# Kernel optimization log

Measured on AMD Instinct MI355X. Metric: run time of the kernel, lower is better.

Reference implementation:

```python
import jax, jax.numpy as jnp
import numpy as np

B, L, D, W = 4, 512, 768, 12
K = L * W  # number of candidate spans


def _mlp(x, w1, b1, w2, b2):
    # Linear -> ReLU -> (Dropout=identity in eval) -> Linear
    return jax.nn.relu(x @ w1.T + b1) @ w2.T + b2


def setup_inputs() -> dict:
    key = jax.random.key(0)
    ks = jax.random.split(key, 16)
    sc_d = 1.0 / np.sqrt(D)
    sc_4d = 1.0 / np.sqrt(4 * D)
    sc_2d = 1.0 / np.sqrt(2 * D)
    inp = {
        "h": jax.random.normal(ks[0], (B, L, D), dtype=jnp.float32),
        "span_idx": jax.random.randint(ks[1], (B, K, 2), 0, L, dtype=jnp.int64),
        # project_start: Linear(D,4D), Linear(4D,D)
        "ws1": jax.random.uniform(ks[2], (4 * D, D), jnp.float32, -sc_d, sc_d),
        "bs1": jax.random.uniform(ks[3], (4 * D,), jnp.float32, -sc_d, sc_d),
        "ws2": jax.random.uniform(ks[4], (D, 4 * D), jnp.float32, -sc_4d, sc_4d),
        "bs2": jax.random.uniform(ks[5], (D,), jnp.float32, -sc_4d, sc_4d),
        # project_end
        "we1": jax.random.uniform(ks[6], (4 * D, D), jnp.float32, -sc_d, sc_d),
        "be1": jax.random.uniform(ks[7], (4 * D,), jnp.float32, -sc_d, sc_d),
        "we2": jax.random.uniform(ks[8], (D, 4 * D), jnp.float32, -sc_4d, sc_4d),
        "be2": jax.random.uniform(ks[9], (D,), jnp.float32, -sc_4d, sc_4d),
        # out_project: Linear(2D,4D), Linear(4D,D)
        "wo1": jax.random.uniform(ks[10], (4 * D, 2 * D), jnp.float32, -sc_2d, sc_2d),
        "bo1": jax.random.uniform(ks[11], (4 * D,), jnp.float32, -sc_2d, sc_2d),
        "wo2": jax.random.uniform(ks[12], (D, 4 * D), jnp.float32, -sc_4d, sc_4d),
        "bo2": jax.random.uniform(ks[13], (D,), jnp.float32, -sc_4d, sc_4d),
    }
    return inp


def reference(h, span_idx, ws1, bs1, ws2, bs2, we1, be1, we2, be2, wo1, bo1, wo2, bo2):
    start_rep = _mlp(h, ws1, bs1, ws2, bs2)  # [B, L, D]
    end_rep = _mlp(h, we1, be1, we2, be2)    # [B, L, D]
    bidx = jnp.arange(B)[:, None]
    start_span = start_rep[bidx, span_idx[:, :, 0]]  # gather along seq dim -> [B, K, D]
    end_span = end_rep[bidx, span_idx[:, :, 1]]      # [B, K, D]
    cat = jax.nn.relu(jnp.concatenate([start_span, end_span], axis=-1))  # [B, K, 2D]
    out = _mlp(cat, wo1, bo1, wo2, bo2)  # [B, K, D]
    return out.reshape(B, L, W, D)
```

## Files before the change

kernel.cpp:

```cpp
#include <hip/hip_runtime.h>
#include <hip/hip_bf16.h>

using bf16 = __hip_bfloat16;
using bf16x8 = __attribute__((ext_vector_type(8))) __bf16;
using f32x4  = __attribute__((ext_vector_type(4))) float;
using u32x4  = __attribute__((ext_vector_type(4))) unsigned;
typedef unsigned short ushort_t;

#define BM 128
#define BN 128
#define BK 32


__device__ __forceinline__ void gl_lds16(const void* g, void* l) {
  __builtin_amdgcn_global_load_lds(
      (const __attribute__((address_space(1))) void*)g,
      (__attribute__((address_space(3))) void*)l, 16, 0, 0);
}

__device__ __forceinline__ ushort_t f2bf(float f) {
  unsigned u = __float_as_uint(f);
  u += 0x7FFF + ((u >> 16) & 1);
  return (ushort_t)(u >> 16);
}

__global__ void sniff(const unsigned* __restrict__ w1,
                      const unsigned* __restrict__ idx, int* flags) {
  __shared__ int cnt[2];
  if (threadIdx.x == 0) { cnt[0] = 0; cnt[1] = 0; }
  __syncthreads();
  int t = threadIdx.x;
  int c0 = 0;
  for (int k = 0; k < 4; ++k) {
    unsigned lo = w1[t * 4 + k] & 0xFFFFu;
    unsigned e = (lo >> 7) & 0xFF;
    if (e <= 122) c0++;
  }
  int c1 = (idx[2 * t + 1] != 0) ? 1 : 0;
  atomicAdd(&cnt[0], c0);
  atomicAdd(&cnt[1], c1);
  __syncthreads();
  if (threadIdx.x == 0) {
    flags[0] = (cnt[0] >= 900) ? 1 : 0;
    flags[1] = (cnt[1] == 0) ? 1 : 0;
  }
}

__global__ void norm_idx(const int* __restrict__ flags, const void* __restrict__ src,
                         int* __restrict__ dst) {
  int i = blockIdx.x * 256 + threadIdx.x;
  int v = flags[1] ? (int)((const long long*)src)[i] : ((const int*)src)[i];
  dst[i] = v;
}

__global__ void cvt_all(const int* __restrict__ flags,
                        const void* s0, const void* s1, const void* s2,
                        const void* s3, const void* s4, const void* s5,
                        const void* s6, ushort_t* __restrict__ dst) {
  long i = ((long)blockIdx.x * 256 + threadIdx.x) * 4;
  const void* src; long off;
  if      (i <  1572864) { src = s0; off = i; }
  else if (i <  3932160) { src = s1; off = i - 1572864; }
  else if (i <  6291456) { src = s2; off = i - 3932160; }
  else if (i <  8650752) { src = s3; off = i - 6291456; }
  else if (i < 11010048) { src = s4; off = i - 8650752; }
  else if (i < 15728640) { src = s5; off = i - 11010048; }
  else                   { src = s6; off = i - 15728640; }
  if (flags[0]) {
    *(ushort4*)(dst + i) = *((const ushort4*)((const ushort_t*)src + off));
  } else {
    float4 f = ((const float4*)src)[off >> 2];
    ushort4 o;
    o.x = f2bf(f.x); o.y = f2bf(f.y); o.z = f2bf(f.z); o.w = f2bf(f.w);
    *(ushort4*)(dst + i) = o;
  }
}

__global__ void cvt_bias(const int* __restrict__ flags,
                         const void* b0, const void* b1, const void* b2,
                         const void* b3, const void* b4, const void* b5,
                         float* __restrict__ dst) {
  int i = blockIdx.x * 256 + threadIdx.x;
  if (i >= 14592) return;
  if (i >= 11520) { dst[i] = 0.f; return; }
  const void* src; int off;
  if (i < 3072)       { src = b0; off = i; }
  else if (i < 3840)  { src = b1; off = i - 3072; }
  else if (i < 6912)  { src = b2; off = i - 3840; }
  else if (i < 7680)  { src = b3; off = i - 6912; }
  else if (i < 10752) { src = b4; off = i - 7680; }
  else                { src = b5; off = i - 10752; }
  dst[i] = flags[0] ? __bfloat162float(((const bf16*)src)[off])
                    : ((const float*)src)[off];
}

template <bool GATHER, bool RELU, bool OUTF32>
__global__ __launch_bounds__(256) void gemm_bt(
    const bf16* __restrict__ A, const bf16* __restrict__ A2,
    const bf16* __restrict__ repS, const bf16* __restrict__ repE,
    const int* __restrict__ sidx, int row_base,
    const bf16* __restrict__ Bw, const bf16* __restrict__ Bw2,
    const float* __restrict__ bias, const float* __restrict__ bias2,
    void* __restrict__ C, void* __restrict__ C2, int nsplit,
    int N, int Kdim, int bstride) {
  __shared__ bf16 lA[BM * BK];
  __shared__ bf16 lB[BN * BK];

  const int tid  = threadIdx.x;
  const int lane = tid & 63;
  const int wave = tid >> 6;
  const int wm = wave >> 1, wn = wave & 1;
  int by = blockIdx.y;
  const bf16* Bw_ = Bw; const float* bias_ = bias; void* C_ = C; const bf16* A_ = A;
  if (by >= nsplit) { by -= nsplit; Bw_ = Bw2; bias_ = bias2; C_ = C2; A_ = A2; }
  const int m0 = blockIdx.x * BM;
  const int n0 = by * BN;

  const int srow = tid >> 2;
  const int scol = 8 * ((tid & 3) ^ ((tid >> 3) & 3));

  const bf16 *a0 = nullptr, *a1 = nullptr;
  const bf16 *pS0 = nullptr, *pE0 = nullptr, *pS1 = nullptr, *pE1 = nullptr;
  if (GATHER) {
    int r0 = row_base + m0 + srow;
    int r1 = r0 + 64;
    int b0 = r0 / 6144, b1 = r1 / 6144;
    int s0 = min(max(sidx[2 * r0], 0), 511);
    int e0 = min(max(sidx[2 * r0 + 1], 0), 511);
    int s1 = min(max(sidx[2 * r1], 0), 511);
    int e1 = min(max(sidx[2 * r1 + 1], 0), 511);
    pS0 = repS + ((size_t)b0 * 512 + s0) * 768 + scol;
    pE0 = repE + ((size_t)b0 * 512 + e0) * 768 + scol;
    pS1 = repS + ((size_t)b1 * 512 + s1) * 768 + scol;
    pE1 = repE + ((size_t)b1 * 512 + e1) * 768 + scol;
  } else {
    a0 = A_ + (size_t)(m0 + srow) * Kdim + scol;
    a1 = a0 + (size_t)64 * Kdim;
  }
  const bf16* b0p = Bw_ + (size_t)(n0 + srow) * bstride + scol;
  const bf16* b1p = b0p + (size_t)64 * bstride;

  f32x4 acc[4][4];
  const f32x4 z = {0.f, 0.f, 0.f, 0.f};
#pragma unroll
  for (int i = 0; i < 4; ++i)
#pragma unroll
    for (int j = 0; j < 4; ++j) acc[i][j] = z;

  const int fr = lane & 15;
  const int fk = 8 * ((lane >> 4) ^ ((lane >> 1) & 3));

  for (int k0 = 0; k0 < Kdim; k0 += BK) {
    const bf16 *sa0, *sa1;
    if (GATHER) {
      if (k0 < 768) { sa0 = pS0 + k0; sa1 = pS1 + k0; }
      else          { sa0 = pE0 + (k0 - 768); sa1 = pE1 + (k0 - 768); }
    } else {
      sa0 = a0 + k0; sa1 = a1 + k0;
    }
    gl_lds16(sa0, lA + tid * 8);
    gl_lds16(sa1, lA + 2048 + tid * 8);
    gl_lds16(b0p + k0, lB + tid * 8);
    gl_lds16(b1p + k0, lB + 2048 + tid * 8);
    __syncthreads();

    bf16x8 af[4], bv[4];
#pragma unroll
    for (int i = 0; i < 4; ++i)
      af[i] = *(const bf16x8*)(const void*)(lA + (wm * 64 + i * 16 + fr) * BK + fk);
#pragma unroll
    for (int j = 0; j < 4; ++j)
      bv[j] = *(const bf16x8*)(const void*)(lB + (wn * 64 + j * 16 + fr) * BK + fk);
#pragma unroll
    for (int i = 0; i < 4; ++i)
#pragma unroll
      for (int j = 0; j < 4; ++j)
        acc[i][j] = __builtin_amdgcn_mfma_f32_16x16x32_bf16(af[i], bv[j], acc[i][j], 0, 0, 0);
    __syncthreads();
  }

  float* Cf = (float*)C_;
  bf16*  Cb = (bf16*)C_;
#pragma unroll
  for (int j = 0; j < 4; ++j) {
    int n = n0 + wn * 64 + j * 16 + fr;
    float bj = bias_[n];
#pragma unroll
    for (int i = 0; i < 4; ++i) {
      int mb = m0 + wm * 64 + i * 16 + (lane >> 4) * 4;
#pragma unroll
      for (int r = 0; r < 4; ++r) {
        float v = acc[i][j][r] + bj;
        if (RELU) v = fmaxf(v, 0.f);
        if (OUTF32) Cf[(size_t)(mb + r) * N + n] = v;
        else        Cb[(size_t)(mb + r) * N + n] = __float2bfloat16(v);
      }
    }
  }
}

__global__ __launch_bounds__(512) void gemm_final_fused(
    const ushort_t* __restrict__ Ps, const ushort_t* __restrict__ Pe,
    const int* __restrict__ sidx,
    const bf16* __restrict__ Bw, const float* __restrict__ bias,
    float* __restrict__ out) {
  __shared__ bf16 lA[2 * 2048];
  __shared__ bf16 lB[2 * 12288];

  const int tid  = threadIdx.x;
  const int lane = tid & 63;
  const int wave = tid >> 6;
  const int m0 = blockIdx.x * 64;
  const int n0 = blockIdx.y * 384;

  const int srow = tid >> 2;
  const int scol = 8 * ((tid & 3) ^ ((tid >> 3) & 3));

  const ushort_t *pS0 = nullptr, *pE0 = nullptr;
  if (tid < 256) {
    int r0 = m0 + srow;
    int b0 = r0 / 6144;
    int s0 = min(max(sidx[2 * r0], 0), 511);
    int e0 = min(max(sidx[2 * r0 + 1], 0), 511);
    pS0 = Ps + ((size_t)b0 * 512 + s0) * 3072 + scol;
    pE0 = Pe + ((size_t)b0 * 512 + e0) * 3072 + scol;
  }
  const bf16* bp0 = Bw + (size_t)(n0 +       srow) * 3072 + scol;
  const bf16* bp1 = Bw + (size_t)(n0 + 128 + srow) * 3072 + scol;
  const bf16* bp2 = Bw + (size_t)(n0 + 256 + srow) * 3072 + scol;

  f32x4 acc[4][3];
  const f32x4 z = {0.f, 0.f, 0.f, 0.f};
#pragma unroll
  for (int i = 0; i < 4; ++i)
#pragma unroll
    for (int j = 0; j < 3; ++j) acc[i][j] = z;

  const int fr = lane & 15;
  const int fk = 8 * ((lane >> 4) ^ ((lane >> 1) & 3));

  auto pack_store = [&](u32x4 xs, u32x4 xe, bf16* dst) {
    u32x4 wv;
#pragma unroll
    for (int q = 0; q < 4; ++q) {
      float lo = fmaxf(__uint_as_float(xs[q] << 16) + __uint_as_float(xe[q] << 16), 0.f);
      float hi = fmaxf(__uint_as_float(xs[q] & 0xFFFF0000u) +
                       __uint_as_float(xe[q] & 0xFFFF0000u), 0.f);
      unsigned w;
      asm("v_cvt_pk_bf16_f32 %0, %1, %2" : "=v"(w) : "v"(lo), "v"(hi));
      wv[q] = w;
    }
    *(u32x4*)(void*)dst = wv;
  };

  {
    gl_lds16(bp0, lB + tid * 8);
    gl_lds16(bp1, lB + 4096 + tid * 8);
    gl_lds16(bp2, lB + 8192 + tid * 8);
    if (tid < 256) {
      u32x4 xs = *(const u32x4*)(const void*)pS0;
      u32x4 xe = *(const u32x4*)(const void*)pE0;
      pack_store(xs, xe, lA + tid * 8);
    }
    __syncthreads();
  }

  for (int it = 0; it < 96; ++it) {
    const int curA = (it & 1) << 11;
    const int curB = (it & 1) * 12288;
    const int nxtA = curA ^ 2048;
    const int nxtB = (curB == 0) ? 12288 : 0;
    const int k1 = (it + 1) * BK;
    const bool pre = (it + 1) < 96;
    u32x4 xs, xe;
    if (pre) {
      gl_lds16(bp0 + k1, lB + nxtB + tid * 8);
      gl_lds16(bp1 + k1, lB + nxtB + 4096 + tid * 8);
      gl_lds16(bp2 + k1, lB + nxtB + 8192 + tid * 8);
      if (tid < 256) {
        xs = *(const u32x4*)(const void*)(pS0 + k1);
        xe = *(const u32x4*)(const void*)(pE0 + k1);
      }
    }

    bf16x8 af[4];
#pragma unroll
    for (int i = 0; i < 4; ++i)
      af[i] = *(const bf16x8*)(const void*)(lA + curA + (i * 16 + fr) * BK + fk);
#pragma unroll
    for (int j = 0; j < 3; ++j) {
      const int nb = wave * 48 + j * 16;
      bf16x8 bv = *(const bf16x8*)(const void*)(
          lB + curB + (nb >> 7) * 4096 + ((nb & 127) + fr) * BK + fk);
#pragma unroll
      for (int i = 0; i < 4; ++i)
        acc[i][j] = __builtin_amdgcn_mfma_f32_16x16x32_bf16(af[i], bv, acc[i][j], 0, 0, 0);
    }

    if (pre && tid < 256) {
      pack_store(xs, xe, lA + nxtA + tid * 8);
    }
    __syncthreads();
  }

#pragma unroll
  for (int j = 0; j < 3; ++j) {
    int n = n0 + wave * 48 + j * 16 + fr;
    float bj = bias[n];
#pragma unroll
    for (int i = 0; i < 4; ++i) {
      int mb = m0 + i * 16 + (lane >> 4) * 4;
#pragma unroll
      for (int r = 0; r < 4; ++r)
        out[(size_t)(mb + r) * 768 + n] = acc[i][j][r] + bj;
    }
  }
}

extern "C" void kernel_launch(void* const* d_in, const int* in_sizes, int n_in,
                              void* d_out, int out_size, void* d_ws, size_t ws_size,
                              hipStream_t stream) {
  const void* h    = d_in[0];
  const void* sidx = d_in[1];
  const void *ws1 = d_in[2],  *bs1 = d_in[3];
  const void *ws2 = d_in[4],  *bs2 = d_in[5];
  const void *we1 = d_in[6],  *be1 = d_in[7];
  const void *we2 = d_in[8],  *be2 = d_in[9];
  const void *wo1 = d_in[10], *bo1 = d_in[11];
  const void *wo2 = d_in[12], *bo2 = d_in[13];

  char* p = (char*)d_ws;
  int*      flags = (int*)p;
  int*      idx32 = (int*)(p + 256);
  float*    biasf = (float*)(p + 256 + 196608);
  ushort_t* hb    = (ushort_t*)(p + 256 + 196608 + 65536);
  ushort_t* w1sb  = hb   + (size_t)1572864;
  ushort_t* w2sb  = w1sb + (size_t)2359296;
  ushort_t* w1eb  = w2sb + (size_t)2359296;
  ushort_t* w2eb  = w1eb + (size_t)2359296;
  ushort_t* wo1b  = w2eb + (size_t)2359296;
  ushort_t* wo2b  = wo1b + (size_t)4718592;
  ushort_t* repS  = wo2b + (size_t)2359296;
  ushort_t* repE  = repS + (size_t)1572864;
  char*     R     = (char*)(repE + (size_t)1572864);
  size_t fixed = (size_t)(R - (char*)d_ws);
  if (ws_size < fixed) return;
  size_t Rsz = ws_size - fixed;

  const size_t P_BF = (size_t)2 * 2048 * 3072 * 2;
  int tier = (Rsz >= P_BF) ? 2 : 3;

  dim3 blk(256);
  const int XBIG = 0x40000000;
  sniff<<<1, blk, 0, stream>>>((const unsigned*)ws1, (const unsigned*)sidx, flags);
  norm_idx<<<192, blk, 0, stream>>>(flags, sidx, idx32);
  cvt_all<<<17664, blk, 0, stream>>>(flags, h, ws1, ws2, we1, we2, wo1, wo2, hb);
  cvt_bias<<<57, blk, 0, stream>>>(flags, bs1, bs2, be1, be2, bo1, bo2, biasf);
  const float *bs1f = biasf, *bs2f = biasf + 3072, *be1f = biasf + 3840,
              *be2f = biasf + 6912, *bo1f = biasf + 7680, *bo2f = biasf + 10752,
              *zerof = biasf + 11520;
  float* outf = (float*)d_out;

  if (tier == 2) {
    ushort_t* hidS = (ushort_t*)R;
    ushort_t* hidE = hidS + (size_t)2048 * 3072;
    gemm_bt<false, true, false><<<dim3(16, 48), blk, 0, stream>>>(
        (const bf16*)hb, (const bf16*)hb, nullptr, nullptr, nullptr, 0,
        (const bf16*)w1sb, (const bf16*)w1eb, bs1f, be1f,
        hidS, hidE, 24, 3072, 768, 768);
    gemm_bt<false, true, false><<<dim3(16, 12), blk, 0, stream>>>(
        (const bf16*)hidS, (const bf16*)hidE, nullptr, nullptr, nullptr, 0,
        (const bf16*)w2sb, (const bf16*)w2eb, bs2f, be2f,
        (bf16*)repS, (bf16*)repE, 6, 768, 3072, 3072);
    ushort_t* Ps = (ushort_t*)R;
    ushort_t* Pe = Ps + (size_t)2048 * 3072;
    gemm_bt<false, false, false><<<dim3(16, 48), blk, 0, stream>>>(
        (const bf16*)repS, (const bf16*)repE, nullptr, nullptr, nullptr, 0,
        (const bf16*)wo1b, (const bf16*)wo1b + 768, bo1f, zerof,
        Ps, Pe, 24, 3072, 768, 1536);
    gemm_final_fused<<<dim3(384, 2), dim3(512), 0, stream>>>(
        Ps, Pe, idx32, (const bf16*)wo2b, bo2f, outf);
  } else {
    long long cT = (long long)(Rsz / ((size_t)2 * 3072 * 2));
    cT = (cT / 128) * 128; if (cT > 2048) cT = 2048;
    long long cO = (long long)(Rsz / ((size_t)3072 * 2));
    cO = (cO / 128) * 128; if (cO > 24576) cO = 24576;
    if (cT < 128 || cO < 128) return;
    ushort_t* scr = (ushort_t*)R;
    for (long long r = 0; r < 2048; r += cT) {
      long long mc = 2048 - r < cT ? 2048 - r : cT;
      ushort_t* hidS = scr;
      ushort_t* hidE = scr + (size_t)cT * 3072;
      gemm_bt<false, true, false><<<dim3(mc / 128, 48), blk, 0, stream>>>(
          (const bf16*)hb + r * 768, (const bf16*)hb + r * 768,
          nullptr, nullptr, nullptr, 0,
          (const bf16*)w1sb, (const bf16*)w1eb, bs1f, be1f,
          hidS, hidE, 24, 3072, 768, 768);
      gemm_bt<false, true, false><<<dim3(mc / 128, 12), blk, 0, stream>>>(
          (const bf16*)hidS, (const bf16*)hidE, nullptr, nullptr, nullptr, 0,
          (const bf16*)w2sb, (const bf16*)w2eb, bs2f, be2f,
          (bf16*)repS + r * 768, (bf16*)repE + r * 768, 6, 768, 3072, 3072);
    }
    for (long long r = 0; r < 24576; r += cO) {
      long long mc = 24576 - r < cO ? 24576 - r : cO;
      gemm_bt<true, true, false><<<dim3(mc / 128, 24), blk, 0, stream>>>(
          nullptr, nullptr, (const bf16*)repS, (const bf16*)repE, idx32, (int)r,
          (const bf16*)wo1b, nullptr, bo1f, nullptr,
          scr, nullptr, XBIG, 3072, 1536, 1536);
      gemm_bt<false, false, true><<<dim3(mc / 128, 6), blk, 0, stream>>>(
          (const bf16*)scr, nullptr, nullptr, nullptr, nullptr, 0,
          (const bf16*)wo2b, nullptr, bo2f, nullptr,
          outf + (size_t)r * 768, nullptr, XBIG, 768, 3072, 3072);
    }
  }
}
```

Before: 485.4 us.

## Retile fused final GEMM to 64x256 tiles with BK=64 and 2x4 wave grid

The gather-fused final GEMM moves from 64x384 block tiles with 8 waves along N to 64x256 tiles with a 2x4 wave layout. Each iteration now covers K=64, split into two 32-wide sub-slabs, which halves the number of loop iterations and barriers. All 512 threads now take part in the gather/ReLU/pack staging of A instead of only half of them. The grid grows to 384x3 blocks. The cost is a larger LDS footprint, and each A row is gathered and converted three times instead of twice.

```diff
diff --git a/kernel.cpp b/kernel.cpp
--- a/kernel.cpp
+++ b/kernel.cpp
@@ -204,37 +204,38 @@
     const int* __restrict__ sidx,
     const bf16* __restrict__ Bw, const float* __restrict__ bias,
     float* __restrict__ out) {
-  __shared__ bf16 lA[2 * 2048];
-  __shared__ bf16 lB[2 * 12288];
+  __shared__ bf16 lA[2 * 4096];
+  __shared__ bf16 lB[2 * 16384];
 
   const int tid  = threadIdx.x;
   const int lane = tid & 63;
   const int wave = tid >> 6;
+  const int wm = wave >> 2, wn = wave & 3;
   const int m0 = blockIdx.x * 64;
-  const int n0 = blockIdx.y * 384;
-
-  const int srow = tid >> 2;
-  const int scol = 8 * ((tid & 3) ^ ((tid >> 3) & 3));
-
-  const ushort_t *pS0 = nullptr, *pE0 = nullptr;
-  if (tid < 256) {
-    int r0 = m0 + srow;
-    int b0 = r0 / 6144;
-    int s0 = min(max(sidx[2 * r0], 0), 511);
-    int e0 = min(max(sidx[2 * r0 + 1], 0), 511);
-    pS0 = Ps + ((size_t)b0 * 512 + s0) * 3072 + scol;
-    pE0 = Pe + ((size_t)b0 * 512 + e0) * 3072 + scol;
-  }
-  const bf16* bp0 = Bw + (size_t)(n0 +       srow) * 3072 + scol;
-  const bf16* bp1 = Bw + (size_t)(n0 + 128 + srow) * 3072 + scol;
-  const bf16* bp2 = Bw + (size_t)(n0 + 256 + srow) * 3072 + scol;
-
-  f32x4 acc[4][3];
+  const int n0 = blockIdx.y * 256;
+
+  const int t8   = tid & 255;
+  const int ksub = tid >> 8;
+  const int srow = t8 >> 2;
+  const int scol = 8 * ((t8 & 3) ^ ((t8 >> 3) & 3));
+
+  int r0 = m0 + srow;
+  int b0 = r0 / 6144;
+  int s0 = min(max(sidx[2 * r0], 0), 511);
+  int e0 = min(max(sidx[2 * r0 + 1], 0), 511);
+  const ushort_t* pS0 = Ps + ((size_t)b0 * 512 + s0) * 3072 + ksub * 32 + scol;
+  const ushort_t* pE0 = Pe + ((size_t)b0 * 512 + e0) * 3072 + ksub * 32 + scol;
+  const int aoff = ksub * 2048 + t8 * 8;
+
+  const bf16* bp = Bw + (size_t)(n0 + srow) * 3072 + ksub * 32 + scol;
+  const int boff = ksub * 8192 + t8 * 8;
+
+  f32x4 acc[2][4];
   const f32x4 z = {0.f, 0.f, 0.f, 0.f};
 #pragma unroll
-  for (int i = 0; i < 4; ++i)
-#pragma unroll
-    for (int j = 0; j < 3; ++j) acc[i][j] = z;
+  for (int i = 0; i < 2; ++i)
+#pragma unroll
+    for (int j = 0; j < 4; ++j) acc[i][j] = z;
 
   const int fr = lane & 15;
   const int fk = 8 * ((lane >> 4) ^ ((lane >> 1) & 3));
@@ -253,63 +254,64 @@
     *(u32x4*)(void*)dst = wv;
   };
 
+  auto stageB = [&](int k0, int buf) {
+#pragma unroll
+    for (int g = 0; g < 4; ++g)
+      gl_lds16(bp + (size_t)g * 64 * 3072 + k0, lB + buf + boff + g * 2048);
+  };
+
   {
-    gl_lds16(bp0, lB + tid * 8);
-    gl_lds16(bp1, lB + 4096 + tid * 8);
-    gl_lds16(bp2, lB + 8192 + tid * 8);
-    if (tid < 256) {
-      u32x4 xs = *(const u32x4*)(const void*)pS0;
-      u32x4 xe = *(const u32x4*)(const void*)pE0;
-      pack_store(xs, xe, lA + tid * 8);
-    }
+    stageB(0, 0);
+    u32x4 xs = *(const u32x4*)(const void*)pS0;
+    u32x4 xe = *(const u32x4*)(const void*)pE0;
+    pack_store(xs, xe, lA + aoff);
     __syncthreads();
   }
 
-  for (int it = 0; it < 96; ++it) {
-    const int curA = (it & 1) << 11;
-    const int curB = (it & 1) * 12288;
-    const int nxtA = curA ^ 2048;
-    const int nxtB = (curB == 0) ? 12288 : 0;
-    const int k1 = (it + 1) * BK;
-    const bool pre = (it + 1) < 96;
+  for (int it = 0; it < 48; ++it) {
+    const int curA = (it & 1) << 12;
+    const int curB = (it & 1) << 14;
+    const int nxtA = curA ^ 4096;
+    const int nxtB = curB ^ 16384;
+    const int k1 = (it + 1) * 64;
+    const bool pre = (it + 1) < 48;
     u32x4 xs, xe;
     if (pre) {
-      gl_lds16(bp0 + k1, lB + nxtB + tid * 8);
-      gl_lds16(bp1 + k1, lB + nxtB + 4096 + tid * 8);
-      gl_lds16(bp2 + k1, lB + nxtB + 8192 + tid * 8);
-      if (tid < 256) {
-        xs = *(const u32x4*)(const void*)(pS0 + k1);
-        xe = *(const u32x4*)(const void*)(pE0 + k1);
+      stageB(k1, nxtB);
+      xs = *(const u32x4*)(const void*)(pS0 + k1);
+      xe = *(const u32x4*)(const void*)(pE0 + k1);
+    }
+
+#pragma unroll
+    for (int s = 0; s < 2; ++s) {
+      bf16x8 af[2];
+#pragma unroll
+      for (int i = 0; i < 2; ++i)
+        af[i] = *(const bf16x8*)(const void*)(
+            lA + curA + s * 2048 + (wm * 32 + i * 16 + fr) * 32 + fk);
+#pragma unroll
+      for (int j = 0; j < 4; ++j) {
+        bf16x8 bv = *(const bf16x8*)(const void*)(
+            lB + curB + s * 8192 + (wn * 64 + j * 16 + fr) * 32 + fk);
+#pragma unroll
+        for (int i = 0; i < 2; ++i)
+          acc[i][j] = __builtin_amdgcn_mfma_f32_16x16x32_bf16(af[i], bv, acc[i][j], 0, 0, 0);
       }
     }
 
-    bf16x8 af[4];
-#pragma unroll
-    for (int i = 0; i < 4; ++i)
-      af[i] = *(const bf16x8*)(const void*)(lA + curA + (i * 16 + fr) * BK + fk);
-#pragma unroll
-    for (int j = 0; j < 3; ++j) {
-      const int nb = wave * 48 + j * 16;
-      bf16x8 bv = *(const bf16x8*)(const void*)(
-          lB + curB + (nb >> 7) * 4096 + ((nb & 127) + fr) * BK + fk);
-#pragma unroll
-      for (int i = 0; i < 4; ++i)
-        acc[i][j] = __builtin_amdgcn_mfma_f32_16x16x32_bf16(af[i], bv, acc[i][j], 0, 0, 0);
-    }
-
-    if (pre && tid < 256) {
-      pack_store(xs, xe, lA + nxtA + tid * 8);
+    if (pre) {
+      pack_store(xs, xe, lA + nxtA + aoff);
     }
     __syncthreads();
   }
 
 #pragma unroll
-  for (int j = 0; j < 3; ++j) {
-    int n = n0 + wave * 48 + j * 16 + fr;
+  for (int j = 0; j < 4; ++j) {
+    int n = n0 + wn * 64 + j * 16 + fr;
     float bj = bias[n];
 #pragma unroll
-    for (int i = 0; i < 4; ++i) {
-      int mb = m0 + i * 16 + (lane >> 4) * 4;
+    for (int i = 0; i < 2; ++i) {
+      int mb = m0 + wm * 32 + i * 16 + (lane >> 4) * 4;
 #pragma unroll
       for (int r = 0; r < 4; ++r)
         out[(size_t)(mb + r) * 768 + n] = acc[i][j][r] + bj;
@@ -378,7 +380,7 @@
         (const bf16*)repS, (const bf16*)repE, nullptr, nullptr, nullptr, 0,
         (const bf16*)wo1b, (const bf16*)wo1b + 768, bo1f, zerof,
         Ps, Pe, 24, 3072, 768, 1536);
-    gemm_final_fused<<<dim3(384, 2), dim3(512), 0, stream>>>(
+    gemm_final_fused<<<dim3(384, 3), dim3(512), 0, stream>>>(
         Ps, Pe, idx32, (const bf16*)wo2b, bo2f, outf);
   } else {
     long long cT = (long long)(Rsz / ((size_t)2 * 3072 * 2));
```

Measured after the change: 494.1 us. Within noise of the previous version (+1.8%).
